# Kernel tuning notes

Hardware: AMD Instinct MI355X
Metric: run time of the kernel (lower is better)

Reference implementation:

```python
import jax, jax.numpy as jnp
import numpy as np
from math import sqrt

MODEL_DIM = 1024
EMBED_DIM = 1024
B, S = 16, 2048


def setup_inputs() -> dict:
    key = jax.random.key(0)
    kq, kk, kv, km, kw, kb = jax.random.split(key, 6)
    Q = jax.random.normal(kq, (B, S, MODEL_DIM), dtype=jnp.float32)
    K = jax.random.normal(kk, (B, S, MODEL_DIM), dtype=jnp.float32)
    # Note: this repo passes V pre-transposed as [B, model_dim, S]
    V = jax.random.normal(kv, (B, MODEL_DIM, S), dtype=jnp.float32)
    attention_mask = jax.random.randint(km, (B, S), 0, 2, dtype=jnp.int32)
    # nn.Linear(model_dim, embed_dim): weight [embed_dim, model_dim], bias [embed_dim]
    W = jax.random.normal(kw, (EMBED_DIM, MODEL_DIM), dtype=jnp.float32) / sqrt(MODEL_DIM)
    b = jax.random.normal(kb, (EMBED_DIM,), dtype=jnp.float32) * 0.01
    return {"Q": Q, "K": K, "V": V, "attention_mask": attention_mask, "W": W, "b": b}


def reference(Q, K, V, attention_mask, W, b):
    lowest = 1e-13  # faithful to original (added to scores; mask fill = -1e-13)
    scale = 1.0 / sqrt(MODEL_DIM)
    # [B,S,S] = Q @ K^T
    score = jnp.einsum("bqd,bkd->bqk", Q, K) * scale + lowest
    # mask key positions (broadcast over query dim), fill with -1e-13 as in source
    score = jnp.where(attention_mask[:, None, :] == 0, -lowest, score)
    attn = jax.nn.softmax(score, axis=2)  # [B,S,S]
    # V is [B, D, S]; V.transpose(1,2) -> [B, S, D]
    result = jnp.einsum("bqk,bdk->bqd", attn, V)  # [B,S,D]
    return result @ W.T + b  # [B,S,embed_dim]
```

## Files before the change

kernel.cpp:

```cpp
#include <hip/hip_runtime.h>

typedef unsigned short u16;
typedef u16 u16x8 __attribute__((ext_vector_type(8)));
typedef float f32x4v __attribute__((ext_vector_type(4)));
typedef __bf16 bf16x8 __attribute__((ext_vector_type(8)));

__device__ __forceinline__ u16 f2bf(float f) {
  unsigned u = __builtin_bit_cast(unsigned, f);
  u += 0x7fffu + ((u >> 16) & 1u);
  return (u16)(u >> 16);
}
__device__ __forceinline__ float bf2f(u16 b) {
  return __builtin_bit_cast(float, (unsigned)b << 16);
}

__global__ __launch_bounds__(256) void cvt_f32_bf16(const float* __restrict__ in,
                                                    u16* __restrict__ out, long n) {
  long i0 = ((long)blockIdx.x * 256 + threadIdx.x) * 8;
  long stride = (long)gridDim.x * 256 * 8;
  for (long i = i0; i < n; i += stride) {
    float4 a = *(const float4*)(in + i);
    float4 b = *(const float4*)(in + i + 4);
    u16x8 o;
    o[0] = f2bf(a.x); o[1] = f2bf(a.y); o[2] = f2bf(a.z); o[3] = f2bf(a.w);
    o[4] = f2bf(b.x); o[5] = f2bf(b.y); o[6] = f2bf(b.z); o[7] = f2bf(b.w);
    *(u16x8*)(out + i) = o;
  }
}

template <int EPI>
__global__ __launch_bounds__(512, 2) void gemm256(
    const u16* __restrict__ A, long lda, long bsA,
    const u16* __restrict__ B, long ldb, long bsB,
    void* __restrict__ Cv, long ldc, long bsC, int K,
    const int* __restrict__ maskp, float scale,
    const float* __restrict__ bias, float* __restrict__ aux) {
  extern __shared__ u16 sm[];
  const int t = threadIdx.x;
  const int lane = t & 63;
  const int w8 = t >> 6;
  const int wr = w8 >> 2;
  const int wc = w8 & 3;

  const int nwg = gridDim.x * gridDim.y * gridDim.z;
  int flat = blockIdx.x + gridDim.x * (blockIdx.y + gridDim.y * blockIdx.z);
  int nid = (flat & 7) * (nwg >> 3) + (flat >> 3);
  const int bx = nid % gridDim.x;
  const int by = (nid / gridDim.x) % gridDim.y;
  const int bz = nid / (gridDim.x * gridDim.y);

  const int sr = t >> 3;
  const int sc = ((t & 7) ^ (sr & 7)) * 8;
  const u16* gA_ = A + (long)bz * bsA + ((long)bx * 256 + sr) * lda + sc;
  const u16* gB_ = B + (long)bz * bsB + ((long)by * 256 + sr) * ldb + sc;

#define GLDS(gptr, lidx)                                                        \
  __builtin_amdgcn_global_load_lds(                                             \
      (const __attribute__((address_space(1))) void*)(gptr),                    \
      (__attribute__((address_space(3))) void*)(sm + (lidx)), 16, 0, 0)

#define STG_A(d, h, kt)                                                         \
  do {                                                                          \
    const int bb = ((d)*2 + (h)) * 8192;                                        \
    const long ko = (long)(kt)*64;                                              \
    GLDS(gA_ + (long)((h)*128) * lda + ko, bb + t * 8);                         \
    GLDS(gA_ + (long)((h)*128 + 64) * lda + ko, bb + 4096 + t * 8);             \
  } while (0)
#define STG_B(d, h, kt)                                                         \
  do {                                                                          \
    const int bb = 32768 + ((d)*2 + (h)) * 8192;                                \
    const long ko = (long)(kt)*64;                                              \
    GLDS(gB_ + (long)((h)*128) * ldb + ko, bb + t * 8);                         \
    GLDS(gB_ + (long)((h)*128 + 64) * ldb + ko, bb + 4096 + t * 8);             \
  } while (0)

  f32x4v acc[8][4];
#pragma unroll
  for (int i = 0; i < 8; ++i)
#pragma unroll
    for (int j = 0; j < 4; ++j) acc[i][j] = (f32x4v){0.f, 0.f, 0.f, 0.f};

  const int g = lane >> 4;
  const int s3 = lane & 7;
  const int rl = lane & 15;
  const int ox0 = ((0 * 4 + g) ^ s3) * 8;
  const int ox1 = ((1 * 4 + g) ^ s3) * 8;
  const int oa0 = rl * 64 + ox0, oa1 = rl * 64 + ox1;
  const int obb = (wc & 1) * 4096 + rl * 64;

  bf16x8 af[4][2], bq[4][2];

#define RD_A(d, rh)                                                             \
  do {                                                                          \
    const int ab = ((d)*2 + wr) * 8192 + (rh)*4096;                             \
    _Pragma("unroll") for (int j = 0; j < 4; ++j) {                             \
      af[j][0] = *(const bf16x8*)(sm + ab + j * 1024 + oa0);                    \
      af[j][1] = *(const bf16x8*)(sm + ab + j * 1024 + oa1);                    \
    }                                                                           \
  } while (0)
#define RD_B(d, ch)                                                             \
  do {                                                                          \
    const int bb = 32768 + ((d)*2 + (wc >> 1)) * 8192 + obb;                    \
    _Pragma("unroll") for (int i = 0; i < 2; ++i) {                             \
      bq[(ch)*2 + i][0] = *(const bf16x8*)(sm + bb + ((ch)*2 + i) * 1024 + ox0);\
      bq[(ch)*2 + i][1] = *(const bf16x8*)(sm + bb + ((ch)*2 + i) * 1024 + ox1);\
    }                                                                           \
  } while (0)
#define DO_MFMA(rh, ch)                                                         \
  do {                                                                          \
    __builtin_amdgcn_s_setprio(1);                                              \
    _Pragma("unroll") for (int j = 0; j < 4; ++j)                               \
        _Pragma("unroll") for (int i = 0; i < 2; ++i) {                         \
      acc[(rh)*4 + j][(ch)*2 + i] = __builtin_amdgcn_mfma_f32_16x16x32_bf16(    \
          af[j][0], bq[(ch)*2 + i][0], acc[(rh)*4 + j][(ch)*2 + i], 0, 0, 0);   \
      acc[(rh)*4 + j][(ch)*2 + i] = __builtin_amdgcn_mfma_f32_16x16x32_bf16(    \
          af[j][1], bq[(ch)*2 + i][1], acc[(rh)*4 + j][(ch)*2 + i], 0, 0, 0);   \
    }                                                                           \
    __builtin_amdgcn_s_setprio(0);                                              \
  } while (0)

#define BAR __builtin_amdgcn_s_barrier()
#define LGKM0                                                                   \
  asm volatile("s_waitcnt lgkmcnt(0)" ::: "memory");                            \
  __builtin_amdgcn_sched_barrier(0)
#define LGKM8 asm volatile("s_waitcnt lgkmcnt(8)" ::: "memory")

  const int nw = K >> 7;

  STG_B(0, 0, 0); STG_B(0, 1, 0);
  STG_A(0, 0, 0); STG_A(0, 1, 0);
  STG_B(1, 0, 1); STG_B(1, 1, 1);
  asm volatile("s_waitcnt vmcnt(4)" ::: "memory");
  BAR;

  for (int w = 0; w < nw; ++w) {
    const int kt1 = 2 * w + 1;
    const bool nx = (w + 1 < nw);
    RD_A(0, 0); RD_B(0, 0);
    STG_A(1, 0, kt1);
    LGKM8; BAR; LGKM0;
    DO_MFMA(0, 0);
    BAR;
    RD_B(0, 1);
    STG_A(1, 1, kt1);
    BAR; LGKM0;
    DO_MFMA(0, 1);
    BAR;
    RD_A(0, 1);
    if (nx) STG_B(0, 0, kt1 + 1);
    BAR; LGKM0;
    DO_MFMA(1, 1);
    BAR;
    if (nx) STG_B(0, 1, kt1 + 1);
    BAR; LGKM0;
    DO_MFMA(1, 0);
    if (nx) asm volatile("s_waitcnt vmcnt(4)" ::: "memory");
    else    asm volatile("s_waitcnt vmcnt(0)" ::: "memory");
    BAR;
    RD_A(1, 0); RD_B(1, 0);
    if (nx) STG_A(0, 0, kt1 + 1);
    LGKM8; BAR; LGKM0;
    DO_MFMA(0, 0);
    BAR;
    RD_B(1, 1);
    if (nx) STG_A(0, 1, kt1 + 1);
    BAR; LGKM0;
    DO_MFMA(0, 1);
    BAR;
    RD_A(1, 1);
    if (nx) STG_B(1, 0, kt1 + 2);
    BAR; LGKM0;
    DO_MFMA(1, 1);
    BAR;
    if (nx) STG_B(1, 1, kt1 + 2);
    BAR; LGKM0;
    DO_MFMA(1, 0);
    if (nx) asm volatile("s_waitcnt vmcnt(4)" ::: "memory");
    BAR;
  }
#undef STG_A
#undef STG_B
#undef GLDS

  const long row0 = (long)bx * 256 + wr * 128;
  const long col0 = (long)by * 256 + wc * 64;
  const int l4 = lane >> 4;
  const int cl = lane & 15;
  if constexpr (EPI == 0) {
    u16* C = (u16*)Cv + (long)bz * bsC;
    const int* mrow = maskp + (long)bz * 2048;
    int mk4[4];
#pragma unroll
    for (int fc = 0; fc < 4; ++fc) mk4[fc] = mrow[col0 + fc * 16 + cl];
#pragma unroll
    for (int fr = 0; fr < 8; ++fr) {
#pragma unroll
      for (int r = 0; r < 4; ++r) {
        long row = row0 + fr * 16 + l4 * 4 + r;
        float s = 0.f;
#pragma unroll
        for (int fc = 0; fc < 4; ++fc) {
          long col = col0 + fc * 16 + cl;
          float e = mk4[fc] ? __expf(acc[fr][fc][r] * scale + 1e-13f) : 1.0f;
          u16 eb = f2bf(e);
          C[row * ldc + col] = eb;
          s += bf2f(eb);
        }
        s += __shfl_xor(s, 1);
        s += __shfl_xor(s, 2);
        s += __shfl_xor(s, 4);
        s += __shfl_xor(s, 8);
        if (cl == 0) aux[((long)bz * 2048 + row) * 32 + by * 4 + wc] = s;
      }
    }
  } else if constexpr (EPI == 1) {
    u16* C = (u16*)Cv + (long)bz * bsC;
    const float* linv = aux + (long)bz * 2048;
#pragma unroll
    for (int fr = 0; fr < 8; ++fr) {
#pragma unroll
      for (int r = 0; r < 4; ++r) {
        long row = row0 + fr * 16 + l4 * 4 + r;
        float li = linv[row];
#pragma unroll
        for (int fc = 0; fc < 4; ++fc) {
          long col = col0 + fc * 16 + cl;
          C[row * ldc + col] = f2bf(acc[fr][fc][r] * li);
        }
      }
    }
  } else {
    float* C = (float*)Cv;
#pragma unroll
    for (int fc = 0; fc < 4; ++fc) {
      long col = col0 + fc * 16 + cl;
      float bj = bias[col];
#pragma unroll
      for (int fr = 0; fr < 8; ++fr) {
        long row = row0 + fr * 16 + l4 * 4;
#pragma unroll
        for (int r = 0; r < 4; ++r) C[(row + r) * ldc + col] = acc[fr][fc][r] + bj;
      }
    }
  }
}

__global__ __launch_bounds__(256) void rowsum_inv(const float* __restrict__ part,
                                                  float* __restrict__ linv) {
  int i = blockIdx.x * 256 + threadIdx.x;
  const float4* p = (const float4*)(part + (long)i * 32);
  float s = 0.f;
#pragma unroll
  for (int j = 0; j < 8; ++j) {
    float4 v = p[j];
    s += (v.x + v.y) + (v.z + v.w);
  }
  linv[i] = 1.0f / s;
}

extern "C" void kernel_launch(void* const* d_in, const int* in_sizes, int n_in,
                              void* d_out, int out_size, void* d_ws, size_t ws_size,
                              hipStream_t stream) {
  const float* Q = (const float*)d_in[0];
  const float* K = (const float*)d_in[1];
  const float* V = (const float*)d_in[2];
  const int* mask = (const int*)d_in[3];
  const float* W = (const float*)d_in[4];
  const float* bias = (const float*)d_in[5];

  const long NQ = 16L * 2048 * 1024;
  u16* Qb = (u16*)d_ws;
  u16* Kb = Qb + NQ;
  u16* Vb = Kb + NQ;
  u16* Wb = Vb + NQ;
  u16* Eb = Wb + 1024L * 1024;
  float* Part = (float*)(Eb + 16L * 2048 * 2048);
  float* Linv = Part + 32768L * 32;
  u16* R = Qb;

  cvt_f32_bf16<<<2048, 256, 0, stream>>>(Q, Qb, NQ);
  cvt_f32_bf16<<<2048, 256, 0, stream>>>(K, Kb, NQ);
  cvt_f32_bf16<<<2048, 256, 0, stream>>>(V, Vb, NQ);
  cvt_f32_bf16<<<512, 256, 0, stream>>>(W, Wb, 1024L * 1024);

  gemm256<0><<<dim3(8, 8, 16), 512, 131072, stream>>>(
      Qb, 1024, 2048L * 1024, Kb, 1024, 2048L * 1024,
      Eb, 2048, 2048L * 2048, 1024, mask, 0.03125f, nullptr, Part);

  rowsum_inv<<<128, 256, 0, stream>>>(Part, Linv);

  gemm256<1><<<dim3(8, 4, 16), 512, 131072, stream>>>(
      Eb, 2048, 2048L * 2048, Vb, 2048, 1024L * 2048,
      R, 1024, 2048L * 1024, 2048, nullptr, 1.f, nullptr, Linv);

  gemm256<2><<<dim3(128, 4, 1), 512, 131072, stream>>>(
      R, 1024, 0, Wb, 1024, 0,
      d_out, 1024, 0, 1024, nullptr, 1.f, bias, nullptr);
}
```

Baseline: 487.6 us.

## Shrink GEMM tile to 128x256 and software-pipeline LDS fragment reads

Result: slower. 582.1 us (+19.4%).

```diff
diff --git a/kernel.cpp b/kernel.cpp
--- a/kernel.cpp
+++ b/kernel.cpp
@@ -29,7 +29,7 @@
 }
 
 template <int EPI>
-__global__ __launch_bounds__(512, 2) void gemm256(
+__global__ __launch_bounds__(512, 2) void gemmRA(
     const u16* __restrict__ A, long lda, long bsA,
     const u16* __restrict__ B, long ldb, long bsB,
     void* __restrict__ Cv, long ldc, long bsC, int K,
@@ -51,7 +51,7 @@
 
   const int sr = t >> 3;
   const int sc = ((t & 7) ^ (sr & 7)) * 8;
-  const u16* gA_ = A + (long)bz * bsA + ((long)bx * 256 + sr) * lda + sc;
+  const u16* gA_ = A + (long)bz * bsA + ((long)bx * 128 + sr) * lda + sc;
   const u16* gB_ = B + (long)bz * bsB + ((long)by * 256 + sr) * ldb + sc;
 
 #define GLDS(gptr, lidx)                                                        \
@@ -59,130 +59,138 @@
       (const __attribute__((address_space(1))) void*)(gptr),                    \
       (__attribute__((address_space(3))) void*)(sm + (lidx)), 16, 0, 0)
 
-#define STG_A(d, h, kt)                                                         \
+#define STGA(d, h, kt)                                                          \
+  GLDS(gA_ + (long)((h)*64) * lda + (long)(kt)*64, ((d)*2 + (h)) * 4096 + t * 8)
+#define STGB(d, h, kt)                                                          \
   do {                                                                          \
-    const int bb = ((d)*2 + (h)) * 8192;                                        \
-    const long ko = (long)(kt)*64;                                              \
-    GLDS(gA_ + (long)((h)*128) * lda + ko, bb + t * 8);                         \
-    GLDS(gA_ + (long)((h)*128 + 64) * lda + ko, bb + 4096 + t * 8);             \
+    const int bb_ = 16384 + ((d)*2 + (h)) * 8192;                               \
+    const long ko_ = (long)(kt)*64;                                             \
+    GLDS(gB_ + (long)((h)*128) * ldb + ko_, bb_ + t * 8);                       \
+    GLDS(gB_ + (long)((h)*128 + 64) * ldb + ko_, bb_ + 4096 + t * 8);           \
   } while (0)
-#define STG_B(d, h, kt)                                                         \
-  do {                                                                          \
-    const int bb = 32768 + ((d)*2 + (h)) * 8192;                                \
-    const long ko = (long)(kt)*64;                                              \
-    GLDS(gB_ + (long)((h)*128) * ldb + ko, bb + t * 8);                         \
-    GLDS(gB_ + (long)((h)*128 + 64) * ldb + ko, bb + 4096 + t * 8);             \
-  } while (0)
-
-  f32x4v acc[8][4];
-#pragma unroll
-  for (int i = 0; i < 8; ++i)
+
+  f32x4v acc[4][4];
+#pragma unroll
+  for (int i = 0; i < 4; ++i)
 #pragma unroll
     for (int j = 0; j < 4; ++j) acc[i][j] = (f32x4v){0.f, 0.f, 0.f, 0.f};
 
   const int g = lane >> 4;
   const int s3 = lane & 7;
   const int rl = lane & 15;
-  const int ox0 = ((0 * 4 + g) ^ s3) * 8;
-  const int ox1 = ((1 * 4 + g) ^ s3) * 8;
-  const int oa0 = rl * 64 + ox0, oa1 = rl * 64 + ox1;
-  const int obb = (wc & 1) * 4096 + rl * 64;
-
-  bf16x8 af[4][2], bq[4][2];
-
-#define RD_A(d, rh)                                                             \
+  const int ox0 = (g ^ s3) * 8;
+  const int ox1 = ((4 + g) ^ s3) * 8;
+  const int aoff = rl * 64;
+  const int boff = (wc & 1) * 4096 + rl * 64;
+
+  bf16x8 afX[2][2], afY[2][2], bq0E[2][2], bq0O[2][2], bq1[2][2];
+
+#define RDA(SET, d, rh)                                                         \
   do {                                                                          \
-    const int ab = ((d)*2 + wr) * 8192 + (rh)*4096;                             \
-    _Pragma("unroll") for (int j = 0; j < 4; ++j) {                             \
-      af[j][0] = *(const bf16x8*)(sm + ab + j * 1024 + oa0);                    \
-      af[j][1] = *(const bf16x8*)(sm + ab + j * 1024 + oa1);                    \
-    }                                                                           \
+    const int ab_ = ((d)*2 + wr) * 4096 + (rh)*2048 + aoff;                     \
+    SET[0][0] = *(const bf16x8*)(sm + ab_ + ox0);                               \
+    SET[0][1] = *(const bf16x8*)(sm + ab_ + ox1);                               \
+    SET[1][0] = *(const bf16x8*)(sm + ab_ + 1024 + ox0);                        \
+    SET[1][1] = *(const bf16x8*)(sm + ab_ + 1024 + ox1);                        \
   } while (0)
-#define RD_B(d, ch)                                                             \
+#define RDB(SET, d, ch)                                                         \
   do {                                                                          \
-    const int bb = 32768 + ((d)*2 + (wc >> 1)) * 8192 + obb;                    \
-    _Pragma("unroll") for (int i = 0; i < 2; ++i) {                             \
-      bq[(ch)*2 + i][0] = *(const bf16x8*)(sm + bb + ((ch)*2 + i) * 1024 + ox0);\
-      bq[(ch)*2 + i][1] = *(const bf16x8*)(sm + bb + ((ch)*2 + i) * 1024 + ox1);\
-    }                                                                           \
+    const int bb_ = 16384 + ((d)*2 + (wc >> 1)) * 8192 + (ch)*2048 + boff;      \
+    SET[0][0] = *(const bf16x8*)(sm + bb_ + ox0);                               \
+    SET[0][1] = *(const bf16x8*)(sm + bb_ + ox1);                               \
+    SET[1][0] = *(const bf16x8*)(sm + bb_ + 1024 + ox0);                        \
+    SET[1][1] = *(const bf16x8*)(sm + bb_ + 1024 + ox1);                        \
   } while (0)
-#define DO_MFMA(rh, ch)                                                         \
+#define MF(rh, ch, AF, BQ)                                                      \
   do {                                                                          \
     __builtin_amdgcn_s_setprio(1);                                              \
-    _Pragma("unroll") for (int j = 0; j < 4; ++j)                               \
+    _Pragma("unroll") for (int j = 0; j < 2; ++j)                               \
         _Pragma("unroll") for (int i = 0; i < 2; ++i) {                         \
-      acc[(rh)*4 + j][(ch)*2 + i] = __builtin_amdgcn_mfma_f32_16x16x32_bf16(    \
-          af[j][0], bq[(ch)*2 + i][0], acc[(rh)*4 + j][(ch)*2 + i], 0, 0, 0);   \
-      acc[(rh)*4 + j][(ch)*2 + i] = __builtin_amdgcn_mfma_f32_16x16x32_bf16(    \
-          af[j][1], bq[(ch)*2 + i][1], acc[(rh)*4 + j][(ch)*2 + i], 0, 0, 0);   \
+      acc[(rh)*2 + j][(ch)*2 + i] = __builtin_amdgcn_mfma_f32_16x16x32_bf16(    \
+          AF[j][0], BQ[i][0], acc[(rh)*2 + j][(ch)*2 + i], 0, 0, 0);            \
+      acc[(rh)*2 + j][(ch)*2 + i] = __builtin_amdgcn_mfma_f32_16x16x32_bf16(    \
+          AF[j][1], BQ[i][1], acc[(rh)*2 + j][(ch)*2 + i], 0, 0, 0);            \
     }                                                                           \
     __builtin_amdgcn_s_setprio(0);                                              \
   } while (0)
 
 #define BAR __builtin_amdgcn_s_barrier()
-#define LGKM0                                                                   \
-  asm volatile("s_waitcnt lgkmcnt(0)" ::: "memory");                            \
+#define LGKM(n)                                                                 \
+  asm volatile("s_waitcnt lgkmcnt(" #n ")" ::: "memory");                       \
   __builtin_amdgcn_sched_barrier(0)
-#define LGKM8 asm volatile("s_waitcnt lgkmcnt(8)" ::: "memory")
+#define VM(n) asm volatile("s_waitcnt vmcnt(" #n ")" ::: "memory")
 
   const int nw = K >> 7;
 
-  STG_B(0, 0, 0); STG_B(0, 1, 0);
-  STG_A(0, 0, 0); STG_A(0, 1, 0);
-  STG_B(1, 0, 1); STG_B(1, 1, 1);
-  asm volatile("s_waitcnt vmcnt(4)" ::: "memory");
+  STGB(0, 0, 0); STGB(0, 1, 0);
+  STGA(0, 0, 0); STGA(0, 1, 0);
+  STGB(1, 0, 1); STGB(1, 1, 1);
+  VM(4);
   BAR;
+  RDA(afX, 0, 0);
+  RDB(bq0E, 0, 0);
 
   for (int w = 0; w < nw; ++w) {
     const int kt1 = 2 * w + 1;
     const bool nx = (w + 1 < nw);
-    RD_A(0, 0); RD_B(0, 0);
-    STG_A(1, 0, kt1);
-    LGKM8; BAR; LGKM0;
-    DO_MFMA(0, 0);
-    BAR;
-    RD_B(0, 1);
-    STG_A(1, 1, kt1);
-    BAR; LGKM0;
-    DO_MFMA(0, 1);
-    BAR;
-    RD_A(0, 1);
-    if (nx) STG_B(0, 0, kt1 + 1);
-    BAR; LGKM0;
-    DO_MFMA(1, 1);
-    BAR;
-    if (nx) STG_B(0, 1, kt1 + 1);
-    BAR; LGKM0;
-    DO_MFMA(1, 0);
-    if (nx) asm volatile("s_waitcnt vmcnt(4)" ::: "memory");
-    else    asm volatile("s_waitcnt vmcnt(0)" ::: "memory");
-    BAR;
-    RD_A(1, 0); RD_B(1, 0);
-    if (nx) STG_A(0, 0, kt1 + 1);
-    LGKM8; BAR; LGKM0;
-    DO_MFMA(0, 0);
-    BAR;
-    RD_B(1, 1);
-    if (nx) STG_A(0, 1, kt1 + 1);
-    BAR; LGKM0;
-    DO_MFMA(0, 1);
-    BAR;
-    RD_A(1, 1);
-    if (nx) STG_B(1, 0, kt1 + 2);
-    BAR; LGKM0;
-    DO_MFMA(1, 1);
-    BAR;
-    if (nx) STG_B(1, 1, kt1 + 2);
-    BAR; LGKM0;
-    DO_MFMA(1, 0);
-    if (nx) asm volatile("s_waitcnt vmcnt(4)" ::: "memory");
+    RDB(bq1, 0, 1);
+    STGA(1, 0, kt1);
+    BAR;
+    LGKM(4);
+    MF(0, 0, afX, bq0E);
+    BAR;
+    RDA(afY, 0, 1);
+    STGA(1, 1, kt1);
+    BAR;
+    LGKM(4);
+    MF(0, 1, afX, bq1);
+    BAR;
+    if (nx) STGB(0, 0, kt1 + 1);
+    BAR;
+    LGKM(0);
+    MF(1, 1, afY, bq1);
+    if (nx) VM(2); else VM(0);
+    BAR;
+    RDA(afX, 1, 0);
+    RDB(bq0O, 1, 0);
+    if (nx) STGB(0, 1, kt1 + 1);
+    BAR;
+    LGKM(8);
+    MF(1, 0, afY, bq0E);
+    BAR;
+    RDB(bq1, 1, 1);
+    if (nx) STGA(0, 0, kt1 + 1);
+    BAR;
+    LGKM(4);
+    MF(0, 0, afX, bq0O);
+    BAR;
+    RDA(afY, 1, 1);
+    if (nx) STGA(0, 1, kt1 + 1);
+    BAR;
+    LGKM(4);
+    MF(0, 1, afX, bq1);
+    BAR;
+    if (nx) STGB(1, 0, kt1 + 2);
+    BAR;
+    LGKM(0);
+    MF(1, 1, afY, bq1);
+    if (nx) VM(2); else VM(0);
+    BAR;
+    if (nx) {
+      RDA(afX, 0, 0);
+      RDB(bq0E, 0, 0);
+      STGB(1, 1, kt1 + 2);
+    }
+    BAR;
+    if (nx) { LGKM(8); } else { LGKM(0); }
+    MF(1, 0, afY, bq0O);
     BAR;
   }
-#undef STG_A
-#undef STG_B
+#undef STGA
+#undef STGB
 #undef GLDS
 
-  const long row0 = (long)bx * 256 + wr * 128;
+  const long row0 = (long)bx * 128 + wr * 64;
   const long col0 = (long)by * 256 + wc * 64;
   const int l4 = lane >> 4;
   const int cl = lane & 15;
@@ -193,7 +201,7 @@
 #pragma unroll
     for (int fc = 0; fc < 4; ++fc) mk4[fc] = mrow[col0 + fc * 16 + cl];
 #pragma unroll
-    for (int fr = 0; fr < 8; ++fr) {
+    for (int fr = 0; fr < 4; ++fr) {
 #pragma unroll
       for (int r = 0; r < 4; ++r) {
         long row = row0 + fr * 16 + l4 * 4 + r;
@@ -217,7 +225,7 @@
     u16* C = (u16*)Cv + (long)bz * bsC;
     const float* linv = aux + (long)bz * 2048;
 #pragma unroll
-    for (int fr = 0; fr < 8; ++fr) {
+    for (int fr = 0; fr < 4; ++fr) {
 #pragma unroll
       for (int r = 0; r < 4; ++r) {
         long row = row0 + fr * 16 + l4 * 4 + r;
@@ -236,7 +244,7 @@
       long col = col0 + fc * 16 + cl;
       float bj = bias[col];
 #pragma unroll
-      for (int fr = 0; fr < 8; ++fr) {
+      for (int fr = 0; fr < 4; ++fr) {
         long row = row0 + fr * 16 + l4 * 4;
 #pragma unroll
         for (int r = 0; r < 4; ++r) C[(row + r) * ldc + col] = acc[fr][fc][r] + bj;
@@ -283,17 +291,17 @@
   cvt_f32_bf16<<<2048, 256, 0, stream>>>(V, Vb, NQ);
   cvt_f32_bf16<<<512, 256, 0, stream>>>(W, Wb, 1024L * 1024);
 
-  gemm256<0><<<dim3(8, 8, 16), 512, 131072, stream>>>(
+  gemmRA<0><<<dim3(16, 8, 16), 512, 98304, stream>>>(
       Qb, 1024, 2048L * 1024, Kb, 1024, 2048L * 1024,
       Eb, 2048, 2048L * 2048, 1024, mask, 0.03125f, nullptr, Part);
 
   rowsum_inv<<<128, 256, 0, stream>>>(Part, Linv);
 
-  gemm256<1><<<dim3(8, 4, 16), 512, 131072, stream>>>(
+  gemmRA<1><<<dim3(16, 4, 16), 512, 98304, stream>>>(
       Eb, 2048, 2048L * 2048, Vb, 2048, 1024L * 2048,
       R, 1024, 2048L * 1024, 2048, nullptr, 1.f, nullptr, Linv);
 
-  gemm256<2><<<dim3(128, 4, 1), 512, 131072, stream>>>(
+  gemmRA<2><<<dim3(256, 4, 1), 512, 98304, stream>>>(
       R, 1024, 0, Wb, 1024, 0,
       d_out, 1024, 0, 1024, nullptr, 1.f, bias, nullptr);
 }
```
